# Kernel optimization log

Measured on AMD Instinct MI355X. Metric: run time of the kernel, lower is better.

## Reference

```python
import jax, jax.numpy as jnp
import numpy as np

K = 4
V = 32000
H = 512
B = 16
SOS = 1
EOS = 2


def setup_inputs() -> dict:
    key = jax.random.key(0)
    ks = jax.random.split(key, 8)
    s = 0.08  # small init keeps GRU/log_softmax well-conditioned
    return {
        "enc_h": jax.random.normal(ks[0], (B, H), jnp.float32),
        "E": jax.random.normal(ks[1], (V, H), jnp.float32) * s,
        "W_ih": jax.random.normal(ks[2], (H, 3 * H), jnp.float32) * s,
        "W_hh": jax.random.normal(ks[3], (H, 3 * H), jnp.float32) * s,
        "b_ih": jax.random.normal(ks[4], (3 * H,), jnp.float32) * s,
        "b_hh": jax.random.normal(ks[5], (3 * H,), jnp.float32) * s,
        "Wo": jax.random.normal(ks[6], (H, V), jnp.float32) * s,
        "bo": jax.random.normal(ks[7], (V,), jnp.float32) * s,
        "max_length": 32,
    }


def _beam_search(enc_h, E, W_ih, W_hh, b_ih, b_hh, Wo, bo, T):
    BK = B * K
    pos = jnp.arange(B, dtype=jnp.int32) * K  # pos_index
    # torch .repeat beam inflation: tiled layout (index i -> original i % B)
    h0 = jnp.tile(enc_h, (K, 1))  # [BK, H]
    inp0 = jnp.full((BK,), SOS, dtype=jnp.int32)
    ss0 = jnp.full((BK,), -jnp.inf, dtype=enc_h.dtype).at[pos].set(0.0)

    def gru(x, h):
        gi = x @ W_ih + b_ih
        gh = h @ W_hh + b_hh
        ir, iz, inn = jnp.split(gi, 3, axis=-1)
        hr, hz, hn = jnp.split(gh, 3, axis=-1)
        r = jax.nn.sigmoid(ir + hr)
        z = jax.nn.sigmoid(iz + hz)
        n = jnp.tanh(inn + r * hn)
        return (1.0 - z) * n + z * h

    def fwd_step(carry, _):
        inp, h, ss = carry
        h_new = gru(E[inp], h)                                   # [BK, H]
        logp = jax.nn.log_softmax(h_new @ Wo + bo, axis=-1)      # [BK, V]
        total = (ss[:, None] + logp).reshape(B, K * V)
        scores, cand = jax.lax.top_k(total, K)                   # [B, K]
        symbols = (cand % V).astype(jnp.int32).reshape(-1)       # input_var
        preds = (cand // V + pos[:, None]).astype(jnp.int32).reshape(-1)
        h_sel = h_new[preds]                                     # index_select hidden
        ss_new = scores.reshape(-1)
        ss_masked = jnp.where(symbols == EOS, -jnp.inf, ss_new)  # EOS masking
        return (symbols, h_sel, ss_masked), (logp, ss_new, preds, symbols, h_sel)

    _, (logps, step_scores, preds, syms, hiddens) = jax.lax.scan(
        fwd_step, (inp0, h0, ss0), None, length=T)

    # ---------------- backtrack ----------------
    last = step_scores[-1].reshape(B, K)
    s0, sorted_idx = jax.lax.top_k(last, K)
    tpred0 = (sorted_idx.astype(jnp.int32) + pos[:, None]).reshape(-1)
    lens0 = jnp.full((B, K), T, dtype=jnp.int32)
    hn0 = jnp.zeros((BK, H), dtype=enc_h.dtype)
    eos0 = jnp.zeros((B,), dtype=jnp.int32)

    def bt_step(carry, xs):
        tpred, eosf, s, lens, hn = carry
        logp_t, hid_t, pred_t, sym_t, score_t, tt = xs
        cur_out = logp_t[tpred]
        cur_hid = hid_t[tpred]
        cur_sym = sym_t[tpred]
        new_pred = pred_t[tpred]
        eos = sym_t == EOS
        eos_bk = eos.reshape(B, K).astype(jnp.int32)
        # original loop processes eos hits in descending beam order per batch
        higher = jnp.cumsum(eos_bk[:, ::-1], axis=1)[:, ::-1] - eos_bk
        occ = eosf[:, None] + higher
        res_k = K - occ % K - 1
        res_flat = (pos[:, None] + res_k).reshape(-1)
        idx = jnp.where(eos, res_flat, BK)  # BK = out of bounds -> dropped
        new_pred = new_pred.at[idx].set(pred_t, mode='drop')
        cur_out = cur_out.at[idx].set(logp_t, mode='drop')
        cur_hid = cur_hid.at[idx].set(hid_t, mode='drop')
        hn = hn.at[idx].set(hid_t, mode='drop')
        cur_sym = cur_sym.at[idx].set(sym_t, mode='drop')
        s = s.reshape(-1).at[idx].set(score_t, mode='drop').reshape(B, K)
        lens = lens.reshape(-1).at[idx].set(tt + 1, mode='drop').reshape(B, K)
        eosf = eosf + eos_bk.sum(axis=1)
        return (new_pred, eosf, s, lens, hn), (cur_out, cur_sym)

    ts = jnp.arange(T - 1, -1, -1, dtype=jnp.int32)
    (_, _, s_fin, lens_fin, hn_fin), (outs_rev, syms_rev) = jax.lax.scan(
        bt_step, (tpred0, eos0, s0, lens0, hn0),
        (logps[::-1], hiddens[::-1], preds[::-1], syms[::-1], step_scores[::-1], ts))

    s_sorted, re_idx = jax.lax.top_k(s_fin, K)
    lens_sorted = jnp.take_along_axis(lens_fin, re_idx, axis=1)
    re_flat = (re_idx.astype(jnp.int32) + pos[:, None]).reshape(-1)
    outs = outs_rev[::-1][:, re_flat].reshape(T, B, K, V)
    seqs = syms_rev[::-1][:, re_flat].reshape(T, B, K)
    decoder_outputs = outs[:, :, 0, :]            # [T, B, V]
    decoder_hidden = hn_fin[re_flat].reshape(B, K, H)[:, 0, :]
    return decoder_outputs, decoder_hidden, s_sorted, lens_sorted, seqs


def reference(enc_h, E, W_ih, W_hh, b_ih, b_hh, Wo, bo, max_length):
    return _beam_search(enc_h, E, W_ih, W_hh, b_ih, b_hh, Wo, bo, int(max_length))
```

## Files before the change

kernel.cpp:

```cpp
#include <hip/hip_runtime.h>
#include <math.h>
#include <limits.h>

#define T_STEPS 32
#define BATCH   16
#define KBEAM   4
#define BKR     64
#define HD      512
#define VOC     32000
#define G3      1536
#define SOS_TOK 1
#define EOS_TOK 2
#define NSP     (VOC/64)
#define NE      (NSP*4)
#define NBG     (G3/64)
#define FMBL    4

#define OFF_HCUR   ((size_t)0)
#define OFF_GBUF   (OFF_HCUR + (size_t)BKR*HD)
#define OFF_HNEW   (OFF_GBUF + (size_t)2*BKR*G3)
#define OFF_LSE    (OFF_HNEW + (size_t)T_STEPS*BKR*HD)
#define OFF_SS     (OFF_LSE + (size_t)T_STEPS*BKR)
#define OFF_SCORES (OFF_SS + BKR)
#define OFF_HNFIN  (OFF_SCORES + (size_t)T_STEPS*BKR)
#define OFF_PV     (OFF_HNFIN + (size_t)BKR*HD)
#define OFF_PM     (OFF_PV + (size_t)BKR*NE)
#define OFF_PS     (OFF_PM + (size_t)BKR*NSP)
#define OFF_FEND   (OFF_PS + (size_t)BKR*NSP)
#define IOFF_INP    0
#define IOFF_PREDS  64
#define IOFF_SYMS   (IOFF_PREDS + T_STEPS*BKR)
#define IOFF_RMAP   (IOFF_SYMS + T_STEPS*BKR)
#define IOFF_PC     (IOFF_RMAP + T_STEPS*BATCH)
#define IOFF_END    (IOFF_PC + BKR*NE)
#define S_WOH   ((size_t)0)
#define S_WOL   (S_WOH + (size_t)NSP*16*2048)
#define S_WGH   (S_WOL + (size_t)NSP*16*2048)
#define S_WGL   (S_WGH + (size_t)2*NBG*16*2048)
#define S_HNH   (S_WGL + (size_t)2*NBG*16*2048)
#define S_HNL   (S_HNH + (size_t)T_STEPS*BKR*HD)
#define S_HCH   (S_HNL + (size_t)T_STEPS*BKR*HD)
#define S_HCL   (S_HCH + (size_t)BKR*HD)
#define S_EIH   (S_HCL + (size_t)BKR*HD)
#define S_EIL   (S_EIH + (size_t)BKR*HD)
#define S_END   (S_EIL + (size_t)BKR*HD)

#define O_HID  ((size_t)T_STEPS*BATCH*VOC)
#define O_SSRT (O_HID + (size_t)BATCH*HD)
#define O_LENS (O_SSRT + BATCH*KBEAM)
#define O_SEQS (O_LENS + BATCH*KBEAM)

typedef short bf16x8 __attribute__((ext_vector_type(8)));
typedef float f32x4  __attribute__((ext_vector_type(4)));

__device__ __forceinline__ unsigned short f2bf(float x){
    unsigned u = __float_as_uint(x);
    return (unsigned short)((u + 0x7fffu + ((u >> 16) & 1u)) >> 16);
}
__device__ __forceinline__ float bf2f(unsigned short h){
    return __uint_as_float(((unsigned)h) << 16);
}

__device__ __forceinline__ void dump_C(f32x4 (&acc)[4], float (&Cs)[64][65], int wave, int lane){
    #pragma unroll
    for (int g = 0; g < 4; ++g){
        int row = g * 16 + (lane >> 4) * 4;
        int col = wave * 16 + (lane & 15);
        #pragma unroll
        for (int r = 0; r < 4; ++r) Cs[row + r][col] = acc[g][r];
    }
}

__device__ __forceinline__ void ins4(float* bv, int* bc, float s, int c){
    bool g0 = (s > bv[0]) || (s == bv[0] && c < bc[0]);
    bool g1 = (s > bv[1]) || (s == bv[1] && c < bc[1]);
    bool g2 = (s > bv[2]) || (s == bv[2] && c < bc[2]);
    bool g3 = (s > bv[3]) || (s == bv[3] && c < bc[3]);
    if (g0){ bv[3]=bv[2];bc[3]=bc[2]; bv[2]=bv[1];bc[2]=bc[1]; bv[1]=bv[0];bc[1]=bc[0]; bv[0]=s; bc[0]=c; }
    else if (g1){ bv[3]=bv[2];bc[3]=bc[2]; bv[2]=bv[1];bc[2]=bc[1]; bv[1]=s; bc[1]=c; }
    else if (g2){ bv[3]=bv[2];bc[3]=bc[2]; bv[2]=s; bc[2]=c; }
    else if (g3){ bv[3]=s; bc[3]=c; }
}


__global__ __launch_bounds__(256) void prepack_kernel(const float* __restrict__ W, int N,
    unsigned short* __restrict__ oh, unsigned short* __restrict__ ol)
{
    const int bx = blockIdx.x, kt = blockIdx.y, tid = threadIdx.x;
    const int bn = tid >> 2, kq = (tid & 3) * 8;
    union { unsigned short u[8]; uint4 v; } h8, l8;
    #pragma unroll
    for (int j = 0; j < 8; ++j){
        float x = W[(size_t)(kt*32 + kq + j) * (size_t)N + bx*64 + bn];
        unsigned short h = f2bf(x);
        h8.u[j] = h; l8.u[j] = f2bf(x - bf2f(h));
    }
    const size_t base = ((size_t)bx*16 + kt) * 2048 + (size_t)tid * 8;
    *(uint4*)(oh + base) = h8.v;
    *(uint4*)(ol + base) = l8.v;
}

__device__ __forceinline__ void mfma_core_pre(
    const unsigned short* __restrict__ ahg, const unsigned short* __restrict__ alg,
    const unsigned short* __restrict__ bth, const unsigned short* __restrict__ btl,
    unsigned short (&Ah)[64][40], unsigned short (&Al)[64][40],
    unsigned short (&Bh)[64][40], unsigned short (&Bl)[64][40],
    f32x4 (&acc)[4])
{
    const int tid = threadIdx.x;
    const int row = tid >> 2, kq = (tid & 3) * 8;
    const int wave = tid >> 6, lane = tid & 63;
    #pragma unroll
    for (int g = 0; g < 4; ++g) acc[g] = (f32x4){0.f, 0.f, 0.f, 0.f};
    for (int kt = 0; kt < 16; ++kt){
        *(uint4*)&Ah[row][kq] = *(const uint4*)(ahg + (size_t)row*512 + kt*32 + kq);
        *(uint4*)&Al[row][kq] = *(const uint4*)(alg + (size_t)row*512 + kt*32 + kq);
        *(uint4*)&Bh[row][kq] = *(const uint4*)(bth + (size_t)kt*2048 + (size_t)tid*8);
        *(uint4*)&Bl[row][kq] = *(const uint4*)(btl + (size_t)kt*2048 + (size_t)tid*8);
        __syncthreads();
        bf16x8 bh = *(const bf16x8*)&Bh[wave*16 + (lane&15)][(lane>>4)*8];
        bf16x8 bl = *(const bf16x8*)&Bl[wave*16 + (lane&15)][(lane>>4)*8];
        #pragma unroll
        for (int g = 0; g < 4; ++g){
            bf16x8 ah = *(const bf16x8*)&Ah[g*16 + (lane&15)][(lane>>4)*8];
            bf16x8 al = *(const bf16x8*)&Al[g*16 + (lane&15)][(lane>>4)*8];
            acc[g] = __builtin_amdgcn_mfma_f32_16x16x32_bf16(ah, bh, acc[g], 0, 0, 0);
            acc[g] = __builtin_amdgcn_mfma_f32_16x16x32_bf16(ah, bl, acc[g], 0, 0, 0);
            acc[g] = __builtin_amdgcn_mfma_f32_16x16x32_bf16(al, bh, acc[g], 0, 0, 0);
        }
        __syncthreads();
    }
}

__global__ __launch_bounds__(256) void gates_pre_kernel(
    const unsigned short* __restrict__ eih, const unsigned short* __restrict__ eil,
    const unsigned short* __restrict__ hch, const unsigned short* __restrict__ hcl,
    const unsigned short* __restrict__ wgh, const unsigned short* __restrict__ wgl,
    const float* __restrict__ b_ih, const float* __restrict__ b_hh,
    float* __restrict__ gbuf)
{
    __shared__ unsigned short Ah[64][40], Al[64][40], Bh[64][40], Bl[64][40];
    __shared__ float Cs[64][65];
    const int z = blockIdx.y, bx = blockIdx.x, n0 = bx * 64;
    const int tid = threadIdx.x;
    const unsigned short* ahg = z ? hch : eih;
    const unsigned short* alg = z ? hcl : eil;
    const size_t bt = ((size_t)z*NBG + bx) * 16 * 2048;
    f32x4 acc[4];
    mfma_core_pre(ahg, alg, wgh + bt, wgl + bt, Ah, Al, Bh, Bl, acc);
    dump_C(acc, Cs, tid >> 6, tid & 63);
    __syncthreads();
    const float* bias = z ? b_hh : b_ih;
    const int row = tid >> 2, c0 = (tid & 3) * 16;
    float* gp = gbuf + (size_t)z * BKR * G3 + (size_t)row * G3 + n0 + c0;
    #pragma unroll
    for (int q = 0; q < 4; ++q){
        float4 bz = *(const float4*)(bias + n0 + c0 + q * 4);
        float4 v;
        v.x = Cs[row][c0 + q*4 + 0] + bz.x;
        v.y = Cs[row][c0 + q*4 + 1] + bz.y;
        v.z = Cs[row][c0 + q*4 + 2] + bz.z;
        v.w = Cs[row][c0 + q*4 + 3] + bz.w;
        *(float4*)(gp + q * 4) = v;
    }
}

__global__ __launch_bounds__(256) void logits_pre_kernel(
    const unsigned short* __restrict__ hnh, const unsigned short* __restrict__ hnl,
    const unsigned short* __restrict__ woh, const unsigned short* __restrict__ wol,
    const float* __restrict__ bo,
    float* __restrict__ pv, int* __restrict__ pc, float* __restrict__ pm, float* __restrict__ ps)
{
    __shared__ unsigned short Ah[64][40], Al[64][40], Bh[64][40], Bl[64][40];
    __shared__ float Cs[64][65];
    const int bx = blockIdx.x, n0 = bx * 64;
    const int tid = threadIdx.x;
    const size_t bt = (size_t)bx * 16 * 2048;
    f32x4 acc[4];
    mfma_core_pre(hnh, hnl, woh + bt, wol + bt, Ah, Al, Bh, Bl, acc);
    dump_C(acc, Cs, tid >> 6, tid & 63);
    __syncthreads();
    const int row = tid >> 2, c0 = (tid & 3) * 16;
    float bv[4] = {-INFINITY,-INFINITY,-INFINITY,-INFINITY};
    int bc[4] = {INT_MAX, INT_MAX, INT_MAX, INT_MAX};
    float m = -INFINITY, s = 0.f;
    #pragma unroll
    for (int j = 0; j < 16; ++j){
        float x = Cs[row][c0 + j] + bo[n0 + c0 + j];
        if (x > m){ s = s * expf(m - x) + 1.f; m = x; }
        else s += expf(x - m);
        ins4(bv, bc, x, n0 + c0 + j);
    }
    #pragma unroll
    for (int o = 1; o < 4; o <<= 1){
        float ov[4]; int oc[4];
        #pragma unroll
        for (int q = 0; q < 4; ++q){ ov[q] = __shfl_xor(bv[q], o); oc[q] = __shfl_xor(bc[q], o); }
        #pragma unroll
        for (int q = 0; q < 4; ++q) ins4(bv, bc, ov[q], oc[q]);
        float m2 = __shfl_xor(m, o), s2 = __shfl_xor(s, o);
        float M = fmaxf(m, m2);
        s = s * expf(m - M) + s2 * expf(m2 - M);
        m = M;
    }
    if ((tid & 3) == 0){
        const size_t base = (size_t)row * NE + (size_t)bx * 4;
        #pragma unroll
        for (int q = 0; q < 4; ++q){ pv[base + q] = bv[q]; pc[base + q] = bc[q]; }
        pm[row * NSP + bx] = m; ps[row * NSP + bx] = s;
    }
}

__global__ __launch_bounds__(256) void final_pre_kernel(
    const unsigned short* __restrict__ hnh, const unsigned short* __restrict__ hnl,
    const int* __restrict__ rmap, const float* __restrict__ lse_all,
    const unsigned short* __restrict__ woh, const unsigned short* __restrict__ wol,
    const float* __restrict__ bo, float* __restrict__ out)
{
    __shared__ unsigned short Ah[64][40], Al[64][40], Bh[64][40], Bl[64][40];
    __shared__ float Cs[64][65];
    __shared__ int sidx[256]; __shared__ float subm[256];
    const int tid = threadIdx.x;
    const int bx = blockIdx.x, n0 = bx * 64;
    const int mbase = blockIdx.y * (64 * FMBL);
    sidx[tid] = rmap[mbase + tid];
    __syncthreads();
    subm[tid] = lse_all[sidx[tid]];
    f32x4 acc[FMBL][4];
    #pragma unroll
    for (int mb = 0; mb < FMBL; ++mb)
        #pragma unroll
        for (int g = 0; g < 4; ++g) acc[mb][g] = (f32x4){0.f, 0.f, 0.f, 0.f};
    const unsigned short* bth = woh + (size_t)bx * 16 * 2048;
    const unsigned short* btl = wol + (size_t)bx * 16 * 2048;
    const int row = tid >> 2, kq = (tid & 3) * 8;
    const int wave = tid >> 6, lane = tid & 63;
    for (int kt = 0; kt < 16; ++kt){
        *(uint4*)&Bh[row][kq] = *(const uint4*)(bth + (size_t)kt*2048 + (size_t)tid*8);
        *(uint4*)&Bl[row][kq] = *(const uint4*)(btl + (size_t)kt*2048 + (size_t)tid*8);
        #pragma unroll
        for (int mb = 0; mb < FMBL; ++mb){
            const int g = sidx[mb*64 + row];
            *(uint4*)&Ah[row][kq] = *(const uint4*)(hnh + (size_t)g*512 + kt*32 + kq);
            *(uint4*)&Al[row][kq] = *(const uint4*)(hnl + (size_t)g*512 + kt*32 + kq);
            __syncthreads();
            bf16x8 bh = *(const bf16x8*)&Bh[wave*16 + (lane&15)][(lane>>4)*8];
            bf16x8 bl = *(const bf16x8*)&Bl[wave*16 + (lane&15)][(lane>>4)*8];
            #pragma unroll
            for (int gg = 0; gg < 4; ++gg){
                bf16x8 ah = *(const bf16x8*)&Ah[gg*16 + (lane&15)][(lane>>4)*8];
                bf16x8 al = *(const bf16x8*)&Al[gg*16 + (lane&15)][(lane>>4)*8];
                acc[mb][gg] = __builtin_amdgcn_mfma_f32_16x16x32_bf16(ah, bh, acc[mb][gg], 0, 0, 0);
                acc[mb][gg] = __builtin_amdgcn_mfma_f32_16x16x32_bf16(ah, bl, acc[mb][gg], 0, 0, 0);
                acc[mb][gg] = __builtin_amdgcn_mfma_f32_16x16x32_bf16(al, bh, acc[mb][gg], 0, 0, 0);
            }
            __syncthreads();
        }
    }
    const int r = tid >> 2, c0 = (tid & 3) * 16;
    #pragma unroll
    for (int mb = 0; mb < FMBL; ++mb){
        dump_C(acc[mb], Cs, wave, lane);
        __syncthreads();
        const float sub = subm[mb*64 + r];
        float* op = out + (size_t)(mbase + mb*64 + r) * VOC + n0 + c0;
        #pragma unroll
        for (int q = 0; q < 4; ++q){
            float4 bz = *(const float4*)(bo + n0 + c0 + q * 4);
            float4 v;
            v.x = Cs[r][c0 + q*4 + 0] + bz.x - sub;
            v.y = Cs[r][c0 + q*4 + 1] + bz.y - sub;
            v.z = Cs[r][c0 + q*4 + 2] + bz.z - sub;
            v.w = Cs[r][c0 + q*4 + 3] + bz.w - sub;
            *(float4*)(op + q * 4) = v;
        }
        __syncthreads();
    }
}

__device__ __forceinline__ void mfma_core(
    const float* __restrict__ Abase, const int* __restrict__ ridx, int mbase,
    const float* __restrict__ B, int ldb, int n0,
    unsigned short (&Ah)[64][40], unsigned short (&Al)[64][40],
    unsigned short (&Bh)[64][40], unsigned short (&Bl)[64][40],
    int (&sidx)[64], f32x4 (&acc)[4])
{
    const int tid = threadIdx.x;
    if (tid < 64) sidx[tid] = ridx ? ridx[mbase + tid] : (mbase + tid);
    #pragma unroll
    for (int g = 0; g < 4; ++g) acc[g] = (f32x4){0.f, 0.f, 0.f, 0.f};
    const int wave = tid >> 6, lane = tid & 63;
    const int am = tid >> 2, ak0 = (tid & 3) * 8;
    const int bn = tid & 63, br0 = (tid >> 6) * 8;
    __syncthreads();
    const float* bcol = B + n0 + bn;
    for (int kt = 0; kt < 16; ++kt){
        {
            const float* ap = Abase + (size_t)sidx[am] * HD + kt * 32 + ak0;
            float4 x0 = *(const float4*)ap, x1 = *(const float4*)(ap + 4);
            float xs[8] = {x0.x, x0.y, x0.z, x0.w, x1.x, x1.y, x1.z, x1.w};
            union { unsigned short u[8]; uint4 v; } h8, l8;
            #pragma unroll
            for (int j = 0; j < 8; ++j){
                unsigned short h = f2bf(xs[j]);
                h8.u[j] = h; l8.u[j] = f2bf(xs[j] - bf2f(h));
            }
            *(uint4*)&Ah[am][ak0] = h8.v;
            *(uint4*)&Al[am][ak0] = l8.v;
        }
        {
            const float* bp = bcol + (size_t)(kt * 32 + br0) * ldb;
            union { unsigned short u[8]; uint4 v; } h8, l8;
            #pragma unroll
            for (int j = 0; j < 8; ++j){
                float x = bp[(size_t)j * ldb];
                unsigned short h = f2bf(x);
                h8.u[j] = h; l8.u[j] = f2bf(x - bf2f(h));
            }
            *(uint4*)&Bh[bn][br0] = h8.v;
            *(uint4*)&Bl[bn][br0] = l8.v;
        }
        __syncthreads();
        bf16x8 bh = *(const bf16x8*)&Bh[wave * 16 + (lane & 15)][(lane >> 4) * 8];
        bf16x8 bl = *(const bf16x8*)&Bl[wave * 16 + (lane & 15)][(lane >> 4) * 8];
        #pragma unroll
        for (int g = 0; g < 4; ++g){
            bf16x8 ah = *(const bf16x8*)&Ah[g * 16 + (lane & 15)][(lane >> 4) * 8];
            bf16x8 al = *(const bf16x8*)&Al[g * 16 + (lane & 15)][(lane >> 4) * 8];
            acc[g] = __builtin_amdgcn_mfma_f32_16x16x32_bf16(ah, bh, acc[g], 0, 0, 0);
            acc[g] = __builtin_amdgcn_mfma_f32_16x16x32_bf16(ah, bl, acc[g], 0, 0, 0);
            acc[g] = __builtin_amdgcn_mfma_f32_16x16x32_bf16(al, bh, acc[g], 0, 0, 0);
        }
        __syncthreads();
    }
}

__global__ __launch_bounds__(256) void gates_mfma_kernel(
    const float* __restrict__ E, const int* __restrict__ inp, const float* __restrict__ h_cur,
    const float* __restrict__ W_ih, const float* __restrict__ W_hh,
    const float* __restrict__ b_ih, const float* __restrict__ b_hh,
    float* __restrict__ gbuf)
{
    __shared__ unsigned short Ah[64][40], Al[64][40], Bh[64][40], Bl[64][40];
    __shared__ int sidx[64];
    __shared__ float Cs[64][65];
    const int z = blockIdx.y;
    const int n0 = blockIdx.x * 64;
    const int tid = threadIdx.x;
    f32x4 acc[4];
    mfma_core(z ? h_cur : E, z ? nullptr : inp, 0,
              z ? W_hh : W_ih, G3, n0, Ah, Al, Bh, Bl, sidx, acc);
    dump_C(acc, Cs, tid >> 6, tid & 63);
    __syncthreads();
    const float* bias = z ? b_hh : b_ih;
    const int row = tid >> 2, c0 = (tid & 3) * 16;
    float* gp = gbuf + (size_t)z * BKR * G3 + (size_t)row * G3 + n0 + c0;
    #pragma unroll
    for (int q = 0; q < 4; ++q){
        float4 bz = *(const float4*)(bias + n0 + c0 + q * 4);
        float4 v;
        v.x = Cs[row][c0 + q*4 + 0] + bz.x;
        v.y = Cs[row][c0 + q*4 + 1] + bz.y;
        v.z = Cs[row][c0 + q*4 + 2] + bz.z;
        v.w = Cs[row][c0 + q*4 + 3] + bz.w;
        *(float4*)(gp + q * 4) = v;
    }
}

__global__ __launch_bounds__(256) void logits_topk_kernel(const float* __restrict__ h_new,
    const float* __restrict__ Wo, const float* __restrict__ bo,
    float* __restrict__ pv, int* __restrict__ pc, float* __restrict__ pm, float* __restrict__ ps)
{
    __shared__ unsigned short Ah[64][40], Al[64][40], Bh[64][40], Bl[64][40];
    __shared__ int sidx[64];
    __shared__ float Cs[64][65];
    const int bx = blockIdx.x, n0 = bx * 64;
    const int tid = threadIdx.x;
    f32x4 acc[4];
    mfma_core(h_new, nullptr, 0, Wo, VOC, n0, Ah, Al, Bh, Bl, sidx, acc);
    dump_C(acc, Cs, tid >> 6, tid & 63);
    __syncthreads();
    const int row = tid >> 2, c0 = (tid & 3) * 16;
    float bv[4] = {-INFINITY,-INFINITY,-INFINITY,-INFINITY};
    int bc[4] = {INT_MAX, INT_MAX, INT_MAX, INT_MAX};
    float m = -INFINITY, s = 0.f;
    #pragma unroll
    for (int j = 0; j < 16; ++j){
        float x = Cs[row][c0 + j] + bo[n0 + c0 + j];
        if (x > m){ s = s * expf(m - x) + 1.f; m = x; }
        else s += expf(x - m);
        ins4(bv, bc, x, n0 + c0 + j);
    }
    #pragma unroll
    for (int o = 1; o < 4; o <<= 1){
        float ov[4]; int oc[4];
        #pragma unroll
        for (int q = 0; q < 4; ++q){ ov[q] = __shfl_xor(bv[q], o); oc[q] = __shfl_xor(bc[q], o); }
        #pragma unroll
        for (int q = 0; q < 4; ++q) ins4(bv, bc, ov[q], oc[q]);
        float m2 = __shfl_xor(m, o), s2 = __shfl_xor(s, o);
        float M = fmaxf(m, m2);
        s = s * expf(m - M) + s2 * expf(m2 - M);
        m = M;
    }
    if ((tid & 3) == 0){
        const size_t base = (size_t)row * NE + (size_t)bx * 4;
        #pragma unroll
        for (int q = 0; q < 4; ++q){ pv[base + q] = bv[q]; pc[base + q] = bc[q]; }
        pm[row * NSP + bx] = m; ps[row * NSP + bx] = s;
    }
}

__global__ __launch_bounds__(256) void final_mfma_kernel(const float* __restrict__ h_new_all,
    const int* __restrict__ rmap, const float* __restrict__ lse_all,
    const float* __restrict__ Wo, const float* __restrict__ bo, float* __restrict__ out)
{
    __shared__ unsigned short Ah[64][40], Al[64][40], Bh[64][40], Bl[64][40];
    __shared__ int sidx[64];
    __shared__ float Cs[64][65];
    __shared__ float subm[64];
    const int n0 = blockIdx.x * 64, mb = blockIdx.y * 64;
    const int tid = threadIdx.x;
    f32x4 acc[4];
    mfma_core(h_new_all, rmap, mb, Wo, VOC, n0, Ah, Al, Bh, Bl, sidx, acc);
    dump_C(acc, Cs, tid >> 6, tid & 63);
    if (tid < 64) subm[tid] = lse_all[sidx[tid]];
    __syncthreads();
    const int row = tid >> 2, c0 = (tid & 3) * 16;
    const float sub = subm[row];
    float* op = out + (size_t)(mb + row) * VOC + n0 + c0;
    #pragma unroll
    for (int q = 0; q < 4; ++q){
        float4 bz = *(const float4*)(bo + n0 + c0 + q * 4);
        float4 v;
        v.x = Cs[row][c0 + q*4 + 0] + bz.x - sub;
        v.y = Cs[row][c0 + q*4 + 1] + bz.y - sub;
        v.z = Cs[row][c0 + q*4 + 2] + bz.z - sub;
        v.w = Cs[row][c0 + q*4 + 3] + bz.w - sub;
        *(float4*)(op + q * 4) = v;
    }
}


__global__ void gru_combine_kernel(const float* __restrict__ gbuf, const float* __restrict__ h_cur,
    float* __restrict__ h_new, unsigned short* __restrict__ hnh, unsigned short* __restrict__ hnl)
{
    int x = blockIdx.x * 256 + threadIdx.x;
    int i = x >> 9, j = x & 511;
    const float* gi = gbuf + (size_t)i * G3;
    const float* gh = gbuf + (size_t)BKR * G3 + (size_t)i * G3;
    float ir = gi[j], iz = gi[j + 512], inn = gi[j + 1024];
    float hr = gh[j], hz = gh[j + 512], hnv = gh[j + 1024];
    float r  = 1.f / (1.f + expf(-(ir + hr)));
    float zz = 1.f / (1.f + expf(-(iz + hz)));
    float n  = tanhf(inn + r * hnv);
    float v = (1.f - zz) * n + zz * h_cur[x];
    h_new[x] = v;
    if (hnh){
        unsigned short h = f2bf(v);
        hnh[x] = h; hnl[x] = f2bf(v - bf2f(h));
    }
}

__global__ __launch_bounds__(256) void topk_phase_b(
    const float* __restrict__ pv, const int* __restrict__ pc,
    const float* __restrict__ pm, const float* __restrict__ ps,
    int t,
    float* __restrict__ scores_all, int* __restrict__ preds_all, int* __restrict__ syms_all,
    float* __restrict__ ss, int* __restrict__ inp, float* __restrict__ lse_all,
    const float* __restrict__ h_new, float* __restrict__ h_cur,
    const float* __restrict__ E,
    unsigned short* __restrict__ hch, unsigned short* __restrict__ hcl,
    unsigned short* __restrict__ eih, unsigned short* __restrict__ eil)
{
    const int b = blockIdx.x, tid = threadIdx.x;
    const int wave = tid >> 6, lane = tid & 63;
    const int row = b * KBEAM + wave;

    float bv[4] = {-INFINITY,-INFINITY,-INFINITY,-INFINITY};
    int bc[4] = {INT_MAX, INT_MAX, INT_MAX, INT_MAX};
    for (int e = lane; e < NE; e += 64)
        ins4(bv, bc, pv[(size_t)row * NE + e], pc[(size_t)row * NE + e]);
    #pragma unroll
    for (int o = 1; o < 64; o <<= 1){
        float ov[4]; int oc[4];
        #pragma unroll
        for (int q = 0; q < 4; ++q){ ov[q] = __shfl_xor(bv[q], o); oc[q] = __shfl_xor(bc[q], o); }
        #pragma unroll
        for (int q = 0; q < 4; ++q) ins4(bv, bc, ov[q], oc[q]);
    }
    float m = -INFINITY, s = 0.f;
    for (int e = lane; e < NSP; e += 64){
        float m2 = pm[row * NSP + e], s2 = ps[row * NSP + e];
        float M = fmaxf(m, m2);
        s = s * expf(m - M) + s2 * expf(m2 - M);
        m = M;
    }
    #pragma unroll
    for (int o = 1; o < 64; o <<= 1){
        float m2 = __shfl_xor(m, o), s2 = __shfl_xor(s, o);
        float M = fmaxf(m, m2);
        s = s * expf(m - M) + s2 * expf(m2 - M);
        m = M;
    }
    __shared__ float rtv[KBEAM][4]; __shared__ int rtc[KBEAM][4];
    __shared__ float rlse[KBEAM];
    if (lane == 0){
        #pragma unroll
        for (int q = 0; q < 4; ++q){ rtv[wave][q] = bv[q]; rtc[wave][q] = bc[q]; }
        rlse[wave] = m + logf(s);
    }
    __syncthreads();
    __shared__ int spred[KBEAM]; __shared__ int ssym[KBEAM];
    if (tid == 0){
        float gv[4] = {-INFINITY,-INFINITY,-INFINITY,-INFINITY};
        int gc[4] = {INT_MAX, INT_MAX, INT_MAX, INT_MAX};
        #pragma unroll
        for (int kl = 0; kl < KBEAM; ++kl){
            const int r2 = b * KBEAM + kl;
            float lse = rlse[kl];
            lse_all[t * BKR + r2] = lse;
            float off = ss[r2] - lse;
            if (off == -INFINITY){
                #pragma unroll
                for (int q = 0; q < 4; ++q) ins4(gv, gc, -INFINITY, kl * VOC + q);
            } else {
                #pragma unroll
                for (int q = 0; q < 4; ++q) ins4(gv, gc, rtv[kl][q] + off, kl * VOC + rtc[kl][q]);
            }
        }
        #pragma unroll
        for (int u = 0; u < KBEAM; ++u){
            int cand = gc[u]; float val = gv[u];
            int sym = cand % VOC; int pg = b * KBEAM + cand / VOC;
            int slot = b * KBEAM + u;
            scores_all[t * BKR + slot] = val;
            syms_all[t * BKR + slot] = sym;
            preds_all[t * BKR + slot] = pg;
            ss[slot] = (sym == EOS_TOK) ? -INFINITY : val;
            inp[slot] = sym;
            spred[u] = pg; ssym[u] = sym;
        }
    }
    __syncthreads();
    for (int x = tid; x < KBEAM * HD; x += 256){
        int u = x >> 9, j = x & 511;
        const int idx = (b * KBEAM + u) * HD + j;
        float v = h_new[spred[u] * HD + j];
        h_cur[idx] = v;
        if (hch){
            unsigned short h = f2bf(v);
            hch[idx] = h; hcl[idx] = f2bf(v - bf2f(h));
            float e = E[(size_t)ssym[u] * HD + j];
            unsigned short eh = f2bf(e);
            eih[idx] = eh; eil[idx] = f2bf(e - bf2f(eh));
        }
    }
}

__global__ void init_kernel(const float* __restrict__ enc_h, const float* __restrict__ E,
    float* __restrict__ h_cur, float* __restrict__ ss, int* __restrict__ inp,
    unsigned short* __restrict__ hch, unsigned short* __restrict__ hcl,
    unsigned short* __restrict__ eih, unsigned short* __restrict__ eil)
{
    const int i = blockIdx.x;
    for (int j = threadIdx.x; j < HD; j += blockDim.x){
        float v = enc_h[(i & (BATCH - 1)) * HD + j];
        h_cur[i * HD + j] = v;
        if (hch){
            const int idx = i * HD + j;
            unsigned short h = f2bf(v);
            hch[idx] = h; hcl[idx] = f2bf(v - bf2f(h));
            float e = E[(size_t)SOS_TOK * HD + j];
            unsigned short eh = f2bf(e);
            eih[idx] = eh; eil[idx] = f2bf(e - bf2f(eh));
        }
    }
    if (i == 0 && threadIdx.x < BKR){
        ss[threadIdx.x] = ((threadIdx.x & (KBEAM - 1)) == 0) ? 0.f : -INFINITY;
        inp[threadIdx.x] = SOS_TOK;
    }
}

__global__ __launch_bounds__(256) void backtrack_kernel(
    const float* __restrict__ scores_all, const int* __restrict__ preds_all, const int* __restrict__ syms_all,
    const float* __restrict__ h_new_all, float* __restrict__ hn_fin,
    int* __restrict__ rmap, float* __restrict__ out)
{
    __shared__ int   l_syms[T_STEPS*BKR];
    __shared__ int   l_preds[T_STEPS*BKR];
    __shared__ float l_scores[T_STEPS*BKR];
    __shared__ int   outrow_s[T_STEPS*BKR];
    __shared__ int   cursym_s[T_STEPS*BKR];
    __shared__ int tpred[64]; __shared__ float sfin[64]; __shared__ int lensq[64];
    __shared__ int eosf[BATCH];
    __shared__ int orow[64], csym[64], npred_s[64];
    __shared__ int cp_slot[64], cp_src[64]; __shared__ int nc_b[BATCH];
    __shared__ int reidx[64];
    const int tid = threadIdx.x;

    for (int x = tid; x < T_STEPS*BKR; x += 256){
        l_syms[x]   = syms_all[x];
        l_preds[x]  = preds_all[x];
        l_scores[x] = scores_all[x];
    }
    for (int x = tid; x < BKR*HD; x += 256) hn_fin[x] = 0.f;
    __syncthreads();

    if (tid < BATCH){
        const int b = tid;
        float v[KBEAM]; int used[KBEAM];
        #pragma unroll
        for (int k = 0; k < KBEAM; ++k){ v[k] = l_scores[(T_STEPS-1)*BKR + b*KBEAM + k]; used[k] = 0; }
        #pragma unroll
        for (int u = 0; u < KBEAM; ++u){
            int best = -1; float bvv = 0.f;
            #pragma unroll
            for (int k = 0; k < KBEAM; ++k) if (!used[k] && (best < 0 || v[k] > bvv)){ best = k; bvv = v[k]; }
            used[best] = 1;
            tpred[b*KBEAM+u] = b*KBEAM + best;
            sfin[b*KBEAM+u] = bvv;
            lensq[b*KBEAM+u] = T_STEPS;
        }
        eosf[b] = 0;
    }
    __syncthreads();

    for (int t = T_STEPS-1; t >= 0; --t){
        if (tid < 64){
            int tp = tpred[tid];
            orow[tid]    = tp;
            csym[tid]    = l_syms[t*BKR + tp];
            npred_s[tid] = l_preds[t*BKR + tp];
        }
        __syncthreads();
        if (tid < BATCH){
            const int b = tid;
            int eos[KBEAM]; int cnt = 0;
            #pragma unroll
            for (int k = 0; k < KBEAM; ++k) eos[k] = (l_syms[t*BKR + b*KBEAM + k] == EOS_TOK);
            int nc = 0;
            #pragma unroll
            for (int k = 0; k < KBEAM; ++k) if (eos[k]){
                int higher = 0;
                #pragma unroll
                for (int k2 = k+1; k2 < KBEAM; ++k2) higher += eos[k2];
                int occ = eosf[b] + higher;
                int rk = KBEAM - (occ % KBEAM) - 1;
                int slot = b*KBEAM + rk;
                int j = b*KBEAM + k;
                npred_s[slot] = l_preds[t*BKR + j];
                orow[slot]    = j;
                csym[slot]    = l_syms[t*BKR + j];
                sfin[slot]    = l_scores[t*BKR + j];
                lensq[slot]   = t + 1;
                cp_slot[b*KBEAM + nc] = slot;
                cp_src[b*KBEAM + nc]  = l_preds[t*BKR + j];
                ++nc; ++cnt;
            }
            nc_b[b] = nc;
            eosf[b] += cnt;
        }
        __syncthreads();
        if (tid < 64){
            outrow_s[t*BKR + tid] = orow[tid];
            cursym_s[t*BKR + tid] = csym[tid];
            tpred[tid] = npred_s[tid];
        }
        {
            const int e = tid >> 2;
            const int eb = e >> 2, eq = e & 3;
            if (eq < nc_b[eb]){
                const int slot = cp_slot[eb*KBEAM + eq];
                const int src  = cp_src[eb*KBEAM + eq];
                const float4* sp = (const float4*)(h_new_all + (size_t)(t*BKR + src)*HD);
                float4* dp = (float4*)(hn_fin + (size_t)slot*HD);
                for (int j = (tid & 3); j < HD/4; j += 4) dp[j] = sp[j];
            }
        }
        __syncthreads();
    }

    if (tid < BATCH){
        const int b = tid;
        float v[KBEAM]; int used[KBEAM];
        #pragma unroll
        for (int k = 0; k < KBEAM; ++k){ v[k] = sfin[b*KBEAM+k]; used[k] = 0; }
        #pragma unroll
        for (int u = 0; u < KBEAM; ++u){
            int best = -1; float bvv = 0.f;
            #pragma unroll
            for (int k = 0; k < KBEAM; ++k) if (!used[k] && (best < 0 || v[k] > bvv)){ best = k; bvv = v[k]; }
            used[best] = 1;
            reidx[b*KBEAM+u] = best;
            out[O_SSRT + b*KBEAM + u] = bvv;
            out[O_LENS + b*KBEAM + u] = (float)lensq[b*KBEAM + best];
        }
    }
    __syncthreads();
    for (int x = tid; x < T_STEPS*BATCH; x += 256){
        int t2 = x >> 4, b = x & 15;
        rmap[x] = t2*BKR + outrow_s[t2*BKR + b*KBEAM + reidx[b*KBEAM]];
    }
    for (int x = tid; x < T_STEPS*BKR; x += 256){
        int t2 = x >> 6, rem = x & 63, b = rem >> 2, k = rem & 3;
        out[O_SEQS + x] = (float)cursym_s[t2*BKR + b*KBEAM + reidx[b*KBEAM + k]];
    }
    for (int x = tid; x < BATCH*HD; x += 256){
        int b = x >> 9, j = x & 511;
        out[O_HID + x] = hn_fin[(b*KBEAM + reidx[b*KBEAM])*HD + j];
    }
}

extern "C" void kernel_launch(void* const* d_in, const int* in_sizes, int n_in,
                              void* d_out, int out_size, void* d_ws, size_t ws_size,
                              hipStream_t stream)
{
    const float* enc_h = (const float*)d_in[0];
    const float* E     = (const float*)d_in[1];
    const float* W_ih  = (const float*)d_in[2];
    const float* W_hh  = (const float*)d_in[3];
    const float* b_ih  = (const float*)d_in[4];
    const float* b_hh  = (const float*)d_in[5];
    const float* Wo    = (const float*)d_in[6];
    const float* bo    = (const float*)d_in[7];
    float* out = (float*)d_out;

    float* w = (float*)d_ws;
    float* h_cur      = w + OFF_HCUR;
    float* gbuf       = w + OFF_GBUF;
    float* h_new_all  = w + OFF_HNEW;
    float* lse_all    = w + OFF_LSE;
    float* ss         = w + OFF_SS;
    float* scores_all = w + OFF_SCORES;
    float* hn_fin     = w + OFF_HNFIN;
    float* pv         = w + OFF_PV;
    float* pm         = w + OFF_PM;
    float* ps         = w + OFF_PS;
    int* wi         = (int*)(w + OFF_FEND);
    int* inp        = wi + IOFF_INP;
    int* preds_all  = wi + IOFF_PREDS;
    int* syms_all   = wi + IOFF_SYMS;
    int* rmap       = wi + IOFF_RMAP;
    int* pc         = wi + IOFF_PC;
    unsigned short* sb = (unsigned short*)(wi + IOFF_END);
    unsigned short* woh = sb + S_WOH;
    unsigned short* wol = sb + S_WOL;
    unsigned short* wgh = sb + S_WGH;
    unsigned short* wgl = sb + S_WGL;
    unsigned short* hnh = sb + S_HNH;
    unsigned short* hnl = sb + S_HNL;
    unsigned short* hch = sb + S_HCH;
    unsigned short* hcl = sb + S_HCL;
    unsigned short* eih = sb + S_EIH;
    unsigned short* eil = sb + S_EIL;

    const size_t NEED = (size_t)OFF_FEND*4 + (size_t)IOFF_END*4 + (size_t)S_END*2;
    const bool pre = (ws_size >= NEED);

    init_kernel<<<dim3(BKR), 256, 0, stream>>>(enc_h, E, h_cur, ss, inp,
        pre ? hch : nullptr, hcl, eih, eil);
    if (pre){
        prepack_kernel<<<dim3(NSP, 16), 256, 0, stream>>>(Wo, VOC, woh, wol);
        prepack_kernel<<<dim3(NBG, 16), 256, 0, stream>>>(W_ih, G3, wgh, wgl);
        prepack_kernel<<<dim3(NBG, 16), 256, 0, stream>>>(W_hh, G3,
            wgh + (size_t)NBG*16*2048, wgl + (size_t)NBG*16*2048);
    }
    for (int t = 0; t < T_STEPS; ++t){
        float* h_new_t = h_new_all + (size_t)t * BKR * HD;
        unsigned short* hnh_t = hnh + (size_t)t * BKR * HD;
        unsigned short* hnl_t = hnl + (size_t)t * BKR * HD;
        if (pre){
            gates_pre_kernel<<<dim3(NBG, 2), 256, 0, stream>>>(eih, eil, hch, hcl,
                wgh, wgl, b_ih, b_hh, gbuf);
        } else {
            gates_mfma_kernel<<<dim3(NBG, 2), 256, 0, stream>>>(E, inp, h_cur, W_ih, W_hh, b_ih, b_hh, gbuf);
        }
        gru_combine_kernel<<<dim3(BKR*HD/256), 256, 0, stream>>>(gbuf, h_cur, h_new_t,
            pre ? hnh_t : nullptr, hnl_t);
        if (pre){
            logits_pre_kernel<<<dim3(NSP), 256, 0, stream>>>(hnh_t, hnl_t, woh, wol, bo, pv, pc, pm, ps);
        } else {
            logits_topk_kernel<<<dim3(NSP), 256, 0, stream>>>(h_new_t, Wo, bo, pv, pc, pm, ps);
        }
        topk_phase_b<<<dim3(BATCH), 256, 0, stream>>>(pv, pc, pm, ps, t, scores_all, preds_all, syms_all,
            ss, inp, lse_all, h_new_t, h_cur, E,
            pre ? hch : nullptr, hcl, eih, eil);
    }
    backtrack_kernel<<<dim3(1), 256, 0, stream>>>(scores_all, preds_all, syms_all, h_new_all, hn_fin,
                                                  rmap, out);
    if (pre){
        final_pre_kernel<<<dim3(NSP, (T_STEPS*BATCH)/(64*FMBL)), 256, 0, stream>>>(
            hnh, hnl, rmap, lse_all, woh, wol, bo, out);
    } else {
        final_mfma_kernel<<<dim3(NSP, T_STEPS*BATCH/64), 256, 0, stream>>>(h_new_all, rmap, lse_all, Wo, bo, out);
    }
}
```

Before: 2.784 ms.

## Double-buffer LDS tiles with register prefetch in bf16-split MFMA GEMM kernels

Rewrites the gates, logits and final-output GEMM kernels to prefetch the next K-tile from global memory into registers while MFMAs run on the current LDS buffer, using two LDS buffers and one barrier per K step. In the final-output kernel all row blocks of A are loaded together per K step instead of one block at a time, and FMBL drops from 4 to 2, halving the accumulators and doubling the grid. The gates and final-output epilogues now write accumulators straight to global memory instead of staging through shared memory, so those stores are strided per lane rather than float4-coalesced. The goal is to hide global-load latency and cut barriers, at the cost of more LDS per block and less reuse of each B tile.

Result: faster. 2.619 ms (-5.9%).

```diff
diff --git a/kernel.cpp b/kernel.cpp
--- a/kernel.cpp
+++ b/kernel.cpp
@@ -14,7 +14,7 @@
 #define NSP     (VOC/64)
 #define NE      (NSP*4)
 #define NBG     (G3/64)
-#define FMBL    4
+#define FMBL    2
 
 #define OFF_HCUR   ((size_t)0)
 #define OFF_GBUF   (OFF_HCUR + (size_t)BKR*HD)
@@ -53,6 +53,8 @@
 typedef short bf16x8 __attribute__((ext_vector_type(8)));
 typedef float f32x4  __attribute__((ext_vector_type(4)));
 
+#define TSZ 2560
+
 __device__ __forceinline__ unsigned short f2bf(float x){
     unsigned u = __float_as_uint(x);
     return (unsigned short)((u + 0x7fffu + ((u >> 16) & 1u)) >> 16);
@@ -61,7 +63,7 @@
     return __uint_as_float(((unsigned)h) << 16);
 }
 
-__device__ __forceinline__ void dump_C(f32x4 (&acc)[4], float (&Cs)[64][65], int wave, int lane){
+__device__ __forceinline__ void dump_C(f32x4 (&acc)[4], float (*Cs)[65], int wave, int lane){
     #pragma unroll
     for (int g = 0; g < 4; ++g){
         int row = g * 16 + (lane >> 4) * 4;
@@ -100,37 +102,6 @@
     *(uint4*)(ol + base) = l8.v;
 }
 
-__device__ __forceinline__ void mfma_core_pre(
-    const unsigned short* __restrict__ ahg, const unsigned short* __restrict__ alg,
-    const unsigned short* __restrict__ bth, const unsigned short* __restrict__ btl,
-    unsigned short (&Ah)[64][40], unsigned short (&Al)[64][40],
-    unsigned short (&Bh)[64][40], unsigned short (&Bl)[64][40],
-    f32x4 (&acc)[4])
-{
-    const int tid = threadIdx.x;
-    const int row = tid >> 2, kq = (tid & 3) * 8;
-    const int wave = tid >> 6, lane = tid & 63;
-    #pragma unroll
-    for (int g = 0; g < 4; ++g) acc[g] = (f32x4){0.f, 0.f, 0.f, 0.f};
-    for (int kt = 0; kt < 16; ++kt){
-        *(uint4*)&Ah[row][kq] = *(const uint4*)(ahg + (size_t)row*512 + kt*32 + kq);
-        *(uint4*)&Al[row][kq] = *(const uint4*)(alg + (size_t)row*512 + kt*32 + kq);
-        *(uint4*)&Bh[row][kq] = *(const uint4*)(bth + (size_t)kt*2048 + (size_t)tid*8);
-        *(uint4*)&Bl[row][kq] = *(const uint4*)(btl + (size_t)kt*2048 + (size_t)tid*8);
-        __syncthreads();
-        bf16x8 bh = *(const bf16x8*)&Bh[wave*16 + (lane&15)][(lane>>4)*8];
-        bf16x8 bl = *(const bf16x8*)&Bl[wave*16 + (lane&15)][(lane>>4)*8];
-        #pragma unroll
-        for (int g = 0; g < 4; ++g){
-            bf16x8 ah = *(const bf16x8*)&Ah[g*16 + (lane&15)][(lane>>4)*8];
-            bf16x8 al = *(const bf16x8*)&Al[g*16 + (lane&15)][(lane>>4)*8];
-            acc[g] = __builtin_amdgcn_mfma_f32_16x16x32_bf16(ah, bh, acc[g], 0, 0, 0);
-            acc[g] = __builtin_amdgcn_mfma_f32_16x16x32_bf16(ah, bl, acc[g], 0, 0, 0);
-            acc[g] = __builtin_amdgcn_mfma_f32_16x16x32_bf16(al, bh, acc[g], 0, 0, 0);
-        }
-        __syncthreads();
-    }
-}
 
 __global__ __launch_bounds__(256) void gates_pre_kernel(
     const unsigned short* __restrict__ eih, const unsigned short* __restrict__ eil,
@@ -139,29 +110,71 @@
     const float* __restrict__ b_ih, const float* __restrict__ b_hh,
     float* __restrict__ gbuf)
 {
-    __shared__ unsigned short Ah[64][40], Al[64][40], Bh[64][40], Bl[64][40];
-    __shared__ float Cs[64][65];
+    __shared__ __align__(16) unsigned short sm[2*4*TSZ];
     const int z = blockIdx.y, bx = blockIdx.x, n0 = bx * 64;
     const int tid = threadIdx.x;
     const unsigned short* ahg = z ? hch : eih;
     const unsigned short* alg = z ? hcl : eil;
     const size_t bt = ((size_t)z*NBG + bx) * 16 * 2048;
+    const unsigned short* bth = wgh + bt;
+    const unsigned short* btl = wgl + bt;
+    const int row = tid >> 2, kq = (tid & 3) * 8;
+    const int wave = tid >> 6, lane = tid & 63;
+    const int fr = lane & 15, fq = lane >> 4;
+    const int wr = row * 40 + kq;
     f32x4 acc[4];
-    mfma_core_pre(ahg, alg, wgh + bt, wgl + bt, Ah, Al, Bh, Bl, acc);
-    dump_C(acc, Cs, tid >> 6, tid & 63);
-    __syncthreads();
+    #pragma unroll
+    for (int g = 0; g < 4; ++g) acc[g] = (f32x4){0.f,0.f,0.f,0.f};
+    {
+        uint4 a_h = *(const uint4*)(ahg + (size_t)row*512 + kq);
+        uint4 a_l = *(const uint4*)(alg + (size_t)row*512 + kq);
+        uint4 b_h = *(const uint4*)(bth + (size_t)tid*8);
+        uint4 b_l = *(const uint4*)(btl + (size_t)tid*8);
+        *(uint4*)(sm + 0*TSZ + wr) = a_h;
+        *(uint4*)(sm + 1*TSZ + wr) = a_l;
+        *(uint4*)(sm + 2*TSZ + wr) = b_h;
+        *(uint4*)(sm + 3*TSZ + wr) = b_l;
+    }
+    __syncthreads();
+    #pragma unroll 2
+    for (int kt = 0; kt < 16; ++kt){
+        unsigned short* cb = sm + (kt & 1) * (4*TSZ);
+        unsigned short* nb = sm + ((kt & 1) ^ 1) * (4*TSZ);
+        uint4 a_h, a_l, b_h, b_l;
+        if (kt < 15){
+            a_h = *(const uint4*)(ahg + (size_t)row*512 + (kt+1)*32 + kq);
+            a_l = *(const uint4*)(alg + (size_t)row*512 + (kt+1)*32 + kq);
+            b_h = *(const uint4*)(bth + (size_t)(kt+1)*2048 + (size_t)tid*8);
+            b_l = *(const uint4*)(btl + (size_t)(kt+1)*2048 + (size_t)tid*8);
+        }
+        bf16x8 bh = *(const bf16x8*)(cb + 2*TSZ + (wave*16 + fr)*40 + fq*8);
+        bf16x8 bl = *(const bf16x8*)(cb + 3*TSZ + (wave*16 + fr)*40 + fq*8);
+        #pragma unroll
+        for (int g = 0; g < 4; ++g){
+            bf16x8 ah = *(const bf16x8*)(cb + 0*TSZ + (g*16 + fr)*40 + fq*8);
+            bf16x8 al = *(const bf16x8*)(cb + 1*TSZ + (g*16 + fr)*40 + fq*8);
+            acc[g] = __builtin_amdgcn_mfma_f32_16x16x32_bf16(ah, bh, acc[g], 0, 0, 0);
+            acc[g] = __builtin_amdgcn_mfma_f32_16x16x32_bf16(ah, bl, acc[g], 0, 0, 0);
+            acc[g] = __builtin_amdgcn_mfma_f32_16x16x32_bf16(al, bh, acc[g], 0, 0, 0);
+        }
+        if (kt < 15){
+            *(uint4*)(nb + 0*TSZ + wr) = a_h;
+            *(uint4*)(nb + 1*TSZ + wr) = a_l;
+            *(uint4*)(nb + 2*TSZ + wr) = b_h;
+            *(uint4*)(nb + 3*TSZ + wr) = b_l;
+        }
+        __syncthreads();
+    }
     const float* bias = z ? b_hh : b_ih;
-    const int row = tid >> 2, c0 = (tid & 3) * 16;
-    float* gp = gbuf + (size_t)z * BKR * G3 + (size_t)row * G3 + n0 + c0;
-    #pragma unroll
-    for (int q = 0; q < 4; ++q){
-        float4 bz = *(const float4*)(bias + n0 + c0 + q * 4);
-        float4 v;
-        v.x = Cs[row][c0 + q*4 + 0] + bz.x;
-        v.y = Cs[row][c0 + q*4 + 1] + bz.y;
-        v.z = Cs[row][c0 + q*4 + 2] + bz.z;
-        v.w = Cs[row][c0 + q*4 + 3] + bz.w;
-        *(float4*)(gp + q * 4) = v;
+    const int col = wave*16 + fr;
+    const float bz = bias[n0 + col];
+    float* gp = gbuf + (size_t)z * BKR * G3 + n0 + col;
+    #pragma unroll
+    for (int g = 0; g < 4; ++g){
+        const int r0 = g*16 + fq*4;
+        #pragma unroll
+        for (int r = 0; r < 4; ++r)
+            gp[(size_t)(r0 + r) * G3] = acc[g][r] + bz;
     }
 }
 
@@ -171,16 +184,62 @@
     const float* __restrict__ bo,
     float* __restrict__ pv, int* __restrict__ pc, float* __restrict__ pm, float* __restrict__ ps)
 {
-    __shared__ unsigned short Ah[64][40], Al[64][40], Bh[64][40], Bl[64][40];
-    __shared__ float Cs[64][65];
+    __shared__ __align__(16) unsigned short sm[2*4*TSZ];
     const int bx = blockIdx.x, n0 = bx * 64;
     const int tid = threadIdx.x;
-    const size_t bt = (size_t)bx * 16 * 2048;
+    const unsigned short* bth = woh + (size_t)bx * 16 * 2048;
+    const unsigned short* btl = wol + (size_t)bx * 16 * 2048;
+    const int row = tid >> 2, kq = (tid & 3) * 8;
+    const int wave = tid >> 6, lane = tid & 63;
+    const int fr = lane & 15, fq = lane >> 4;
+    const int wr = row * 40 + kq;
     f32x4 acc[4];
-    mfma_core_pre(hnh, hnl, woh + bt, wol + bt, Ah, Al, Bh, Bl, acc);
-    dump_C(acc, Cs, tid >> 6, tid & 63);
-    __syncthreads();
-    const int row = tid >> 2, c0 = (tid & 3) * 16;
+    #pragma unroll
+    for (int g = 0; g < 4; ++g) acc[g] = (f32x4){0.f,0.f,0.f,0.f};
+    {
+        uint4 a_h = *(const uint4*)(hnh + (size_t)row*512 + kq);
+        uint4 a_l = *(const uint4*)(hnl + (size_t)row*512 + kq);
+        uint4 b_h = *(const uint4*)(bth + (size_t)tid*8);
+        uint4 b_l = *(const uint4*)(btl + (size_t)tid*8);
+        *(uint4*)(sm + 0*TSZ + wr) = a_h;
+        *(uint4*)(sm + 1*TSZ + wr) = a_l;
+        *(uint4*)(sm + 2*TSZ + wr) = b_h;
+        *(uint4*)(sm + 3*TSZ + wr) = b_l;
+    }
+    __syncthreads();
+    #pragma unroll 2
+    for (int kt = 0; kt < 16; ++kt){
+        unsigned short* cb = sm + (kt & 1) * (4*TSZ);
+        unsigned short* nb = sm + ((kt & 1) ^ 1) * (4*TSZ);
+        uint4 a_h, a_l, b_h, b_l;
+        if (kt < 15){
+            a_h = *(const uint4*)(hnh + (size_t)row*512 + (kt+1)*32 + kq);
+            a_l = *(const uint4*)(hnl + (size_t)row*512 + (kt+1)*32 + kq);
+            b_h = *(const uint4*)(bth + (size_t)(kt+1)*2048 + (size_t)tid*8);
+            b_l = *(const uint4*)(btl + (size_t)(kt+1)*2048 + (size_t)tid*8);
+        }
+        bf16x8 bh = *(const bf16x8*)(cb + 2*TSZ + (wave*16 + fr)*40 + fq*8);
+        bf16x8 bl = *(const bf16x8*)(cb + 3*TSZ + (wave*16 + fr)*40 + fq*8);
+        #pragma unroll
+        for (int g = 0; g < 4; ++g){
+            bf16x8 ah = *(const bf16x8*)(cb + 0*TSZ + (g*16 + fr)*40 + fq*8);
+            bf16x8 al = *(const bf16x8*)(cb + 1*TSZ + (g*16 + fr)*40 + fq*8);
+            acc[g] = __builtin_amdgcn_mfma_f32_16x16x32_bf16(ah, bh, acc[g], 0, 0, 0);
+            acc[g] = __builtin_amdgcn_mfma_f32_16x16x32_bf16(ah, bl, acc[g], 0, 0, 0);
+            acc[g] = __builtin_amdgcn_mfma_f32_16x16x32_bf16(al, bh, acc[g], 0, 0, 0);
+        }
+        if (kt < 15){
+            *(uint4*)(nb + 0*TSZ + wr) = a_h;
+            *(uint4*)(nb + 1*TSZ + wr) = a_l;
+            *(uint4*)(nb + 2*TSZ + wr) = b_h;
+            *(uint4*)(nb + 3*TSZ + wr) = b_l;
+        }
+        __syncthreads();
+    }
+    float (*Cs)[65] = (float(*)[65])sm;
+    dump_C(acc, Cs, wave, lane);
+    __syncthreads();
+    const int c0 = (tid & 3) * 16;
     float bv[4] = {-INFINITY,-INFINITY,-INFINITY,-INFINITY};
     int bc[4] = {INT_MAX, INT_MAX, INT_MAX, INT_MAX};
     float m = -INFINITY, s = 0.f;
@@ -217,64 +276,90 @@
     const unsigned short* __restrict__ woh, const unsigned short* __restrict__ wol,
     const float* __restrict__ bo, float* __restrict__ out)
 {
-    __shared__ unsigned short Ah[64][40], Al[64][40], Bh[64][40], Bl[64][40];
-    __shared__ float Cs[64][65];
-    __shared__ int sidx[256]; __shared__ float subm[256];
+    __shared__ __align__(16) unsigned short sm[2*6*TSZ];
+    __shared__ int sidx[64*FMBL]; __shared__ float subm[64*FMBL];
     const int tid = threadIdx.x;
     const int bx = blockIdx.x, n0 = bx * 64;
     const int mbase = blockIdx.y * (64 * FMBL);
-    sidx[tid] = rmap[mbase + tid];
-    __syncthreads();
-    subm[tid] = lse_all[sidx[tid]];
-    f32x4 acc[FMBL][4];
-    #pragma unroll
-    for (int mb = 0; mb < FMBL; ++mb)
-        #pragma unroll
-        for (int g = 0; g < 4; ++g) acc[mb][g] = (f32x4){0.f, 0.f, 0.f, 0.f};
+    if (tid < 64*FMBL){ int g = rmap[mbase + tid]; sidx[tid] = g; subm[tid] = lse_all[g]; }
+    __syncthreads();
+    const int row = tid >> 2, kq = (tid & 3) * 8;
+    const int wave = tid >> 6, lane = tid & 63;
+    const int fr = lane & 15, fq = lane >> 4;
+    const int wr = row * 40 + kq;
+    const size_t r0 = (size_t)sidx[row] * 512;
+    const size_t r1 = (size_t)sidx[64 + row] * 512;
     const unsigned short* bth = woh + (size_t)bx * 16 * 2048;
     const unsigned short* btl = wol + (size_t)bx * 16 * 2048;
-    const int row = tid >> 2, kq = (tid & 3) * 8;
-    const int wave = tid >> 6, lane = tid & 63;
+    f32x4 acc[FMBL][4];
+    #pragma unroll
+    for (int mb = 0; mb < FMBL; ++mb)
+        #pragma unroll
+        for (int g = 0; g < 4; ++g) acc[mb][g] = (f32x4){0.f,0.f,0.f,0.f};
+    {
+        uint4 a0h = *(const uint4*)(hnh + r0 + kq);
+        uint4 a0l = *(const uint4*)(hnl + r0 + kq);
+        uint4 a1h = *(const uint4*)(hnh + r1 + kq);
+        uint4 a1l = *(const uint4*)(hnl + r1 + kq);
+        uint4 b_h = *(const uint4*)(bth + (size_t)tid*8);
+        uint4 b_l = *(const uint4*)(btl + (size_t)tid*8);
+        *(uint4*)(sm + 0*TSZ + wr) = a0h;
+        *(uint4*)(sm + 1*TSZ + wr) = a0l;
+        *(uint4*)(sm + 2*TSZ + wr) = a1h;
+        *(uint4*)(sm + 3*TSZ + wr) = a1l;
+        *(uint4*)(sm + 4*TSZ + wr) = b_h;
+        *(uint4*)(sm + 5*TSZ + wr) = b_l;
+    }
+    __syncthreads();
+    #pragma unroll 2
     for (int kt = 0; kt < 16; ++kt){
-        *(uint4*)&Bh[row][kq] = *(const uint4*)(bth + (size_t)kt*2048 + (size_t)tid*8);
-        *(uint4*)&Bl[row][kq] = *(const uint4*)(btl + (size_t)kt*2048 + (size_t)tid*8);
+        unsigned short* cb = sm + (kt & 1) * (6*TSZ);
+        unsigned short* nb = sm + ((kt & 1) ^ 1) * (6*TSZ);
+        uint4 a0h, a0l, a1h, a1l, b_h, b_l;
+        if (kt < 15){
+            a0h = *(const uint4*)(hnh + r0 + (kt+1)*32 + kq);
+            a0l = *(const uint4*)(hnl + r0 + (kt+1)*32 + kq);
+            a1h = *(const uint4*)(hnh + r1 + (kt+1)*32 + kq);
+            a1l = *(const uint4*)(hnl + r1 + (kt+1)*32 + kq);
+            b_h = *(const uint4*)(bth + (size_t)(kt+1)*2048 + (size_t)tid*8);
+            b_l = *(const uint4*)(btl + (size_t)(kt+1)*2048 + (size_t)tid*8);
+        }
+        bf16x8 bh = *(const bf16x8*)(cb + 4*TSZ + (wave*16 + fr)*40 + fq*8);
+        bf16x8 bl = *(const bf16x8*)(cb + 5*TSZ + (wave*16 + fr)*40 + fq*8);
         #pragma unroll
         for (int mb = 0; mb < FMBL; ++mb){
-            const int g = sidx[mb*64 + row];
-            *(uint4*)&Ah[row][kq] = *(const uint4*)(hnh + (size_t)g*512 + kt*32 + kq);
-            *(uint4*)&Al[row][kq] = *(const uint4*)(hnl + (size_t)g*512 + kt*32 + kq);
-            __syncthreads();
-            bf16x8 bh = *(const bf16x8*)&Bh[wave*16 + (lane&15)][(lane>>4)*8];
-            bf16x8 bl = *(const bf16x8*)&Bl[wave*16 + (lane&15)][(lane>>4)*8];
             #pragma unroll
-            for (int gg = 0; gg < 4; ++gg){
-                bf16x8 ah = *(const bf16x8*)&Ah[gg*16 + (lane&15)][(lane>>4)*8];
-                bf16x8 al = *(const bf16x8*)&Al[gg*16 + (lane&15)][(lane>>4)*8];
-                acc[mb][gg] = __builtin_amdgcn_mfma_f32_16x16x32_bf16(ah, bh, acc[mb][gg], 0, 0, 0);
-                acc[mb][gg] = __builtin_amdgcn_mfma_f32_16x16x32_bf16(ah, bl, acc[mb][gg], 0, 0, 0);
-                acc[mb][gg] = __builtin_amdgcn_mfma_f32_16x16x32_bf16(al, bh, acc[mb][gg], 0, 0, 0);
+            for (int g = 0; g < 4; ++g){
+                bf16x8 ah = *(const bf16x8*)(cb + (2*mb+0)*TSZ + (g*16 + fr)*40 + fq*8);
+                bf16x8 al = *(const bf16x8*)(cb + (2*mb+1)*TSZ + (g*16 + fr)*40 + fq*8);
+                acc[mb][g] = __builtin_amdgcn_mfma_f32_16x16x32_bf16(ah, bh, acc[mb][g], 0, 0, 0);
+                acc[mb][g] = __builtin_amdgcn_mfma_f32_16x16x32_bf16(ah, bl, acc[mb][g], 0, 0, 0);
+                acc[mb][g] = __builtin_amdgcn_mfma_f32_16x16x32_bf16(al, bh, acc[mb][g], 0, 0, 0);
             }
-            __syncthreads();
-        }
-    }
-    const int r = tid >> 2, c0 = (tid & 3) * 16;
+        }
+        if (kt < 15){
+            *(uint4*)(nb + 0*TSZ + wr) = a0h;
+            *(uint4*)(nb + 1*TSZ + wr) = a0l;
+            *(uint4*)(nb + 2*TSZ + wr) = a1h;
+            *(uint4*)(nb + 3*TSZ + wr) = a1l;
+            *(uint4*)(nb + 4*TSZ + wr) = b_h;
+            *(uint4*)(nb + 5*TSZ + wr) = b_l;
+        }
+        __syncthreads();
+    }
+    const int col = n0 + wave*16 + fr;
+    const float bz = bo[col];
     #pragma unroll
     for (int mb = 0; mb < FMBL; ++mb){
-        dump_C(acc[mb], Cs, wave, lane);
-        __syncthreads();
-        const float sub = subm[mb*64 + r];
-        float* op = out + (size_t)(mbase + mb*64 + r) * VOC + n0 + c0;
-        #pragma unroll
-        for (int q = 0; q < 4; ++q){
-            float4 bz = *(const float4*)(bo + n0 + c0 + q * 4);
-            float4 v;
-            v.x = Cs[r][c0 + q*4 + 0] + bz.x - sub;
-            v.y = Cs[r][c0 + q*4 + 1] + bz.y - sub;
-            v.z = Cs[r][c0 + q*4 + 2] + bz.z - sub;
-            v.w = Cs[r][c0 + q*4 + 3] + bz.w - sub;
-            *(float4*)(op + q * 4) = v;
-        }
-        __syncthreads();
+        #pragma unroll
+        for (int g = 0; g < 4; ++g){
+            const int rb = mb*64 + g*16 + fq*4;
+            #pragma unroll
+            for (int r = 0; r < 4; ++r){
+                const int rowi = rb + r;
+                out[(size_t)(mbase + rowi) * VOC + col] = acc[mb][g][r] + bz - subm[rowi];
+            }
+        }
     }
 }
 
```
